# Optimization experiments

Hardware: AMD Instinct MI355X
Metric: run time of the kernel (lower is better)

Reference implementation:

```python
import jax, jax.numpy as jnp
import numpy as np

B, YS, XS, H = 16, 256, 256, 128  # batch, image height (y_size), width (x_size), MLP hidden


def setup_inputs() -> dict:
    key = jax.random.key(0)
    ks = jax.random.split(key, 6)
    images = jax.random.normal(ks[0], (B, YS, XS), dtype=jnp.float32)

    def glorot(k, shape):
        fan_in = shape[0]
        return (jax.random.normal(k, shape, dtype=jnp.float32) / np.float32(np.sqrt(fan_in)))

    W1 = glorot(ks[1], (3, H));  b1 = jnp.zeros((H,), jnp.float32)
    W2 = glorot(ks[2], (H, H));  b2 = jnp.zeros((H,), jnp.float32)
    W3 = glorot(ks[3], (H, H));  b3 = jnp.zeros((H,), jnp.float32)
    W4 = glorot(ks[4], (H, 1));  b4 = jnp.zeros((1,), jnp.float32)
    return {
        "images": images,
        "W1": W1, "b1": b1, "W2": W2, "b2": b2,
        "W3": W3, "b3": b3, "W4": W4, "b4": b4,
        "diffusion_weight": jnp.float32(0.1),
        "n": 0,
    }


def reference(images, W1, b1, W2, b2, W3, b3, W4, b4, diffusion_weight, n):
    # NOTE: in the original torch module, diffusion_loss (and all autograd
    # derivatives) are computed but never added to total_loss; only
    # boundary_loss accumulates. We reproduce exactly that math.
    Bn, y_size, x_size = images.shape
    x = jnp.linspace(-x_size / 2, x_size / 2, x_size, dtype=images.dtype)
    y = jnp.linspace(-y_size / 2, y_size / 2, y_size, dtype=images.dtype)
    Xg, Yg = jnp.meshgrid(x, y, indexing="ij")  # (x_size, y_size), x-major
    xf = Xg.ravel()  # (N,) with N = x_size*y_size
    yf = Yg.ravel()

    # t_recon is all-zeros in the original, so T_recon_i = i + n*B (constant field).
    ts = jnp.arange(Bn, dtype=images.dtype) + jnp.asarray(n * Bn, images.dtype)  # (B,)

    def field(tval):
        tf = jnp.zeros_like(xf) + tval
        inp = jnp.stack([xf, yf, tf], axis=-1)          # (N, 3)
        h = jnp.tanh(inp @ W1 + b1)
        h = jnp.tanh(h @ W2 + b2)
        h = jnp.tanh(h @ W3 + b3)
        return (h @ W4 + b4)[:, 0]                       # (N,)

    surface_recon = jax.vmap(field)(ts)                  # (B, N)
    # matches torch: surface_recon.view(y_size, x_size) on the ij-flattened field
    recon = surface_recon.reshape(Bn, y_size, x_size)
    boundary = jnp.mean((images - recon) ** 2, axis=(1, 2))  # per-sample
    return jnp.sum(boundary) / Bn
```

## Files before the change

### kernel.cpp

```cpp
#include <hip/hip_runtime.h>
#include <hip/hip_bf16.h>


#define BATCH 16
#define LDA 136
#define STEP (256.0f / 255.0f)
#define KS 2.8853900817779268f

typedef __bf16 v8bf __attribute__((ext_vector_type(8)));
typedef float  v4f  __attribute__((ext_vector_type(4)));

__device__ __forceinline__ unsigned short f2bf(float f) {
    unsigned int u = __float_as_uint(f);
    unsigned int r = (u + 0x7fffu + ((u >> 16) & 1u)) >> 16;
    return (unsigned short)r;
}

#if __has_builtin(__builtin_amdgcn_perm)
__device__ __forceinline__ unsigned int pack2bf(float a, float b) {
    return __builtin_amdgcn_perm(__float_as_uint(b), __float_as_uint(a), 0x07060302u);
}
#else
__device__ __forceinline__ unsigned int pack2bf(float a, float b) {
    return (__float_as_uint(a) >> 16) | (__float_as_uint(b) & 0xffff0000u);
}
#endif

__device__ __forceinline__ float tanh_pre(float zk) {
    float e = __builtin_amdgcn_exp2f(zk);
    float r = __builtin_amdgcn_rcpf(e + 1.f);
    return fmaf(-2.f, r, 1.f);
}

__global__ __launch_bounds__(256) void prep_kernel(
    const float* __restrict__ W2, const float* __restrict__ W3,
    unsigned short* __restrict__ w2t, unsigned short* __restrict__ w3t,
    float* __restrict__ partials, unsigned int* __restrict__ counter)
{
    int o = blockIdx.x * 256 + threadIdx.x;
    if (o < 1024) partials[o] = 0.f;
    if (o == 0) *counter = 0u;
    const float* src = (o < 16384) ? W2 : W3;
    unsigned short* dst = (o < 16384) ? w2t : w3t;
    int e = o & 16383;
    int k = e >> 7, n = e & 127;
    dst[n * 128 + k] = f2bf(src[e] * KS);
}

__global__ __launch_bounds__(512, 8) void main_kernel(
    const float* __restrict__ images,
    const float* __restrict__ W1, const float* __restrict__ b1,
    const float* __restrict__ b2, const float* __restrict__ b3,
    const float* __restrict__ W4, const float* __restrict__ b4,
    const int*   __restrict__ np,
    const unsigned short* __restrict__ w2t,
    const unsigned short* __restrict__ w3t,
    float* __restrict__ partials, unsigned int* __restrict__ counter,
    float* __restrict__ out)
{
    __shared__ unsigned short A[128 * LDA];
    __shared__ float P[8][128];
    __shared__ float red[8];
    __shared__ unsigned int isLastS;

    const int tid  = threadIdx.x;
    const int lane = tid & 63;
    const int w    = tid >> 6;
    const int l15  = lane & 15;
    const int quad = lane >> 4;

    const int bid = blockIdx.x;
    const int b   = bid >> 9;
    const int rem = bid & 511;
    const int r   = rem >> 1;
    const int c0  = (rem & 1) << 7;

    const float tv = (float)(b + np[0] * BATCH);
    const float xv = -128.f + (float)r * STEP;

    {
        const int lo = tid & 31, hi = tid >> 5;
        const int j0 = lo * 4, p0 = hi * 8;
        float4 wx = *(const float4*)(W1 + j0);
        float4 wy = *(const float4*)(W1 + 128 + j0);
        float4 wt = *(const float4*)(W1 + 256 + j0);
        float4 bb = *(const float4*)(b1 + j0);
        float wy0 = KS * wy.x, wy1 = KS * wy.y, wy2 = KS * wy.z, wy3 = KS * wy.w;
        const float yv0 = fmaf((float)(c0 + p0), STEP, -128.f);
        float z0 = fmaf(yv0, wy0, KS * fmaf(xv, wx.x, fmaf(tv, wt.x, bb.x)));
        float z1 = fmaf(yv0, wy1, KS * fmaf(xv, wx.y, fmaf(tv, wt.y, bb.y)));
        float z2 = fmaf(yv0, wy2, KS * fmaf(xv, wx.z, fmaf(tv, wt.z, bb.z)));
        float z3 = fmaf(yv0, wy3, KS * fmaf(xv, wx.w, fmaf(tv, wt.w, bb.w)));
        const float d0 = STEP * wy0, d1 = STEP * wy1, d2 = STEP * wy2, d3 = STEP * wy3;
        #pragma unroll
        for (int pi = 0; pi < 8; ++pi) {
            uint2 u = make_uint2(pack2bf(tanh_pre(z0), tanh_pre(z1)),
                                 pack2bf(tanh_pre(z2), tanh_pre(z3)));
            *(uint2*)&A[(p0 + pi) * LDA + j0] = u;
            z0 += d0; z1 += d1; z2 += d2; z3 += d3;
        }
    }
    __syncthreads();

    const int colw = w * 16 + l15;
    const int ch4  = w * 16 + quad * 4;

    v8bf wf[4];
    #pragma unroll
    for (int ks = 0; ks < 4; ++ks)
        wf[ks] = *(const v8bf*)(w2t + colw * 128 + ks * 32 + quad * 8);

    v4f acc[8];
    {
        float4 b2q = *(const float4*)(b2 + ch4);
        v4f ini = (v4f){b2q.x * KS, b2q.y * KS, b2q.z * KS, b2q.w * KS};
        #pragma unroll
        for (int mt = 0; mt < 8; ++mt) acc[mt] = ini;
    }
    #pragma unroll
    for (int ks = 0; ks < 4; ++ks) {
        #pragma unroll
        for (int mt = 0; mt < 8; ++mt) {
            v8bf af = *(const v8bf*)&A[(mt * 16 + l15) * LDA + ks * 32 + quad * 8];
            acc[mt] = __builtin_amdgcn_mfma_f32_16x16x32_bf16(wf[ks], af, acc[mt], 0, 0, 0);
        }
    }

    #pragma unroll
    for (int ks = 0; ks < 4; ++ks)
        wf[ks] = *(const v8bf*)(w3t + colw * 128 + ks * 32 + quad * 8);
    __syncthreads();

    #pragma unroll
    for (int mt = 0; mt < 8; ++mt) {
        uint2 u = make_uint2(pack2bf(tanh_pre(acc[mt][0]), tanh_pre(acc[mt][1])),
                             pack2bf(tanh_pre(acc[mt][2]), tanh_pre(acc[mt][3])));
        *(uint2*)&A[(mt * 16 + l15) * LDA + ch4] = u;
    }
    __syncthreads();

    {
        float4 b3q = *(const float4*)(b3 + ch4);
        v4f ini = (v4f){b3q.x * KS, b3q.y * KS, b3q.z * KS, b3q.w * KS};
        #pragma unroll
        for (int mt = 0; mt < 8; ++mt) acc[mt] = ini;
    }
    #pragma unroll
    for (int ks = 0; ks < 4; ++ks) {
        #pragma unroll
        for (int mt = 0; mt < 8; ++mt) {
            v8bf af = *(const v8bf*)&A[(mt * 16 + l15) * LDA + ks * 32 + quad * 8];
            acc[mt] = __builtin_amdgcn_mfma_f32_16x16x32_bf16(wf[ks], af, acc[mt], 0, 0, 0);
        }
    }

    {
        float4 w4q = *(const float4*)(W4 + ch4);
        #pragma unroll
        for (int mt = 0; mt < 8; ++mt) {
            float s;
            s  = tanh_pre(acc[mt][0]) * w4q.x;
            s  = fmaf(tanh_pre(acc[mt][1]), w4q.y, s);
            s  = fmaf(tanh_pre(acc[mt][2]), w4q.z, s);
            s  = fmaf(tanh_pre(acc[mt][3]), w4q.w, s);
            s += __shfl_xor(s, 16, 64);
            s += __shfl_xor(s, 32, 64);
            if (quad == 0) P[w][mt * 16 + l15] = s;
        }
    }
    __syncthreads();

    {
        float e2 = 0.f;
        if (tid < 128) {
            float s = b4[0];
            #pragma unroll
            for (int ww = 0; ww < 8; ++ww) s += P[ww][tid];
            float img = images[(b << 16) + (r << 8) + c0 + tid];
            float err = img - s;
            e2 = err * err;
        }
        #pragma unroll
        for (int off = 1; off < 64; off <<= 1)
            e2 += __shfl_xor(e2, off, 64);
        if (lane == 0 && tid < 128)
            atomicAdd(&partials[bid & 1023], e2);
    }

    __syncthreads();
    if (tid == 0)
        isLastS = (atomicAdd(counter, 1u) == (unsigned)(gridDim.x - 1)) ? 1u : 0u;
    __syncthreads();
    if (isLastS) {
        float s = __hip_atomic_load(&partials[tid],       __ATOMIC_RELAXED, __HIP_MEMORY_SCOPE_AGENT)
                + __hip_atomic_load(&partials[tid + 512], __ATOMIC_RELAXED, __HIP_MEMORY_SCOPE_AGENT);
        #pragma unroll
        for (int off = 1; off < 64; off <<= 1)
            s += __shfl_xor(s, off, 64);
        if (lane == 0) red[w] = s;
        __syncthreads();
        if (tid == 0) {
            float tot = 0.f;
            #pragma unroll
            for (int i = 0; i < 8; ++i) tot += red[i];
            out[0] = tot * (1.f / 1048576.f);
        }
    }
}

extern "C" void kernel_launch(void* const* d_in, const int* in_sizes, int n_in,
                              void* d_out, int out_size, void* d_ws, size_t ws_size,
                              hipStream_t stream)
{
    const float* images = (const float*)d_in[0];
    const float* W1 = (const float*)d_in[1];
    const float* b1 = (const float*)d_in[2];
    const float* W2 = (const float*)d_in[3];
    const float* b2 = (const float*)d_in[4];
    const float* W3 = (const float*)d_in[5];
    const float* b3 = (const float*)d_in[6];
    const float* W4 = (const float*)d_in[7];
    const float* b4 = (const float*)d_in[8];
    const int*   np = (const int*)d_in[10];

    unsigned short* w2t = (unsigned short*)d_ws;
    unsigned short* w3t = w2t + 128 * 128;
    float* partials = (float*)((char*)d_ws + 65536);
    unsigned int* counter = (unsigned int*)((char*)d_ws + 65536 + 4096);

    prep_kernel<<<128, 256, 0, stream>>>(W2, W3, w2t, w3t, partials, counter);
    main_kernel<<<BATCH * 256 * 2, 512, 0, stream>>>(
        images, W1, b1, b2, b3, W4, b4, np, w2t, w3t, partials, counter, (float*)d_out);
}
```

Baseline: 200.6 us.

## Switch hidden-layer GEMMs to 32x32x16 MFMA with 2D wave tiling

After: 235.1 us. 1.17x slower.

```diff
diff --git a/kernel.cpp b/kernel.cpp
--- a/kernel.cpp
+++ b/kernel.cpp
@@ -8,7 +8,7 @@
 #define KS 2.8853900817779268f
 
 typedef __bf16 v8bf __attribute__((ext_vector_type(8)));
-typedef float  v4f  __attribute__((ext_vector_type(4)));
+typedef float  v16f __attribute__((ext_vector_type(16)));
 
 __device__ __forceinline__ unsigned short f2bf(float f) {
     unsigned int u = __float_as_uint(f);
@@ -59,15 +59,18 @@
     float* __restrict__ out)
 {
     __shared__ unsigned short A[128 * LDA];
-    __shared__ float P[8][128];
+    __shared__ float P[4][128];
     __shared__ float red[8];
     __shared__ unsigned int isLastS;
 
     const int tid  = threadIdx.x;
     const int lane = tid & 63;
     const int w    = tid >> 6;
-    const int l15  = lane & 15;
-    const int quad = lane >> 4;
+    const int i32  = lane & 31;
+    const int h    = lane >> 5;
+
+    const int chb  = (w & 3) * 32;
+    const int ptb  = (w >> 2) * 64;
 
     const int bid = blockIdx.x;
     const int b   = bid >> 9;
@@ -102,70 +105,103 @@
     }
     __syncthreads();
 
-    const int colw = w * 16 + l15;
-    const int ch4  = w * 16 + quad * 4;
-
-    v8bf wf[4];
+    const int ch0 = chb + 4 * h;
+
+    const unsigned short* wb2 = w2t + (chb + i32) * 128 + h * 8;
+    v16f acc0, acc1;
+    {
+        float4 g0 = *(const float4*)(b2 + ch0);
+        float4 g1 = *(const float4*)(b2 + ch0 + 8);
+        float4 g2 = *(const float4*)(b2 + ch0 + 16);
+        float4 g3 = *(const float4*)(b2 + ch0 + 24);
+        acc0 = (v16f){g0.x*KS, g0.y*KS, g0.z*KS, g0.w*KS,
+                      g1.x*KS, g1.y*KS, g1.z*KS, g1.w*KS,
+                      g2.x*KS, g2.y*KS, g2.z*KS, g2.w*KS,
+                      g3.x*KS, g3.y*KS, g3.z*KS, g3.w*KS};
+        acc1 = acc0;
+    }
+    {
+        v8bf wcur = *(const v8bf*)(wb2);
+        #pragma unroll
+        for (int ks = 0; ks < 8; ++ks) {
+            v8bf wnext = (ks < 7) ? *(const v8bf*)(wb2 + (ks + 1) * 16) : wcur;
+            v8bf af0 = *(const v8bf*)&A[(ptb + i32)      * LDA + ks * 16 + h * 8];
+            v8bf af1 = *(const v8bf*)&A[(ptb + 32 + i32) * LDA + ks * 16 + h * 8];
+            acc0 = __builtin_amdgcn_mfma_f32_32x32x16_bf16(wcur, af0, acc0, 0, 0, 0);
+            acc1 = __builtin_amdgcn_mfma_f32_32x32x16_bf16(wcur, af1, acc1, 0, 0, 0);
+            wcur = wnext;
+        }
+    }
+    __syncthreads();
+
     #pragma unroll
-    for (int ks = 0; ks < 4; ++ks)
-        wf[ks] = *(const v8bf*)(w2t + colw * 128 + ks * 32 + quad * 8);
-
-    v4f acc[8];
-    {
-        float4 b2q = *(const float4*)(b2 + ch4);
-        v4f ini = (v4f){b2q.x * KS, b2q.y * KS, b2q.z * KS, b2q.w * KS};
-        #pragma unroll
-        for (int mt = 0; mt < 8; ++mt) acc[mt] = ini;
-    }
-    #pragma unroll
-    for (int ks = 0; ks < 4; ++ks) {
-        #pragma unroll
-        for (int mt = 0; mt < 8; ++mt) {
-            v8bf af = *(const v8bf*)&A[(mt * 16 + l15) * LDA + ks * 32 + quad * 8];
-            acc[mt] = __builtin_amdgcn_mfma_f32_16x16x32_bf16(wf[ks], af, acc[mt], 0, 0, 0);
-        }
-    }
-
-    #pragma unroll
-    for (int ks = 0; ks < 4; ++ks)
-        wf[ks] = *(const v8bf*)(w3t + colw * 128 + ks * 32 + quad * 8);
-    __syncthreads();
-
-    #pragma unroll
-    for (int mt = 0; mt < 8; ++mt) {
-        uint2 u = make_uint2(pack2bf(tanh_pre(acc[mt][0]), tanh_pre(acc[mt][1])),
-                             pack2bf(tanh_pre(acc[mt][2]), tanh_pre(acc[mt][3])));
-        *(uint2*)&A[(mt * 16 + l15) * LDA + ch4] = u;
-    }
-    __syncthreads();
-
-    {
-        float4 b3q = *(const float4*)(b3 + ch4);
-        v4f ini = (v4f){b3q.x * KS, b3q.y * KS, b3q.z * KS, b3q.w * KS};
-        #pragma unroll
-        for (int mt = 0; mt < 8; ++mt) acc[mt] = ini;
-    }
-    #pragma unroll
-    for (int ks = 0; ks < 4; ++ks) {
-        #pragma unroll
-        for (int mt = 0; mt < 8; ++mt) {
-            v8bf af = *(const v8bf*)&A[(mt * 16 + l15) * LDA + ks * 32 + quad * 8];
-            acc[mt] = __builtin_amdgcn_mfma_f32_16x16x32_bf16(wf[ks], af, acc[mt], 0, 0, 0);
-        }
-    }
-
-    {
-        float4 w4q = *(const float4*)(W4 + ch4);
-        #pragma unroll
-        for (int mt = 0; mt < 8; ++mt) {
+    for (int t = 0; t < 2; ++t) {
+        const v16f& ac = t ? acc1 : acc0;
+        const int prow = (ptb + t * 32 + i32) * LDA;
+        #pragma unroll
+        for (int g = 0; g < 4; ++g) {
+            float t0 = tanh_pre(ac[4 * g + 0]);
+            float t1 = tanh_pre(ac[4 * g + 1]);
+            float t2 = tanh_pre(ac[4 * g + 2]);
+            float t3 = tanh_pre(ac[4 * g + 3]);
+            uint2 u = make_uint2(pack2bf(t0, t1), pack2bf(t2, t3));
+            *(uint2*)&A[prow + ch0 + 8 * g] = u;
+        }
+    }
+    __syncthreads();
+
+    const unsigned short* wb3 = w3t + (chb + i32) * 128 + h * 8;
+    {
+        float4 g0 = *(const float4*)(b3 + ch0);
+        float4 g1 = *(const float4*)(b3 + ch0 + 8);
+        float4 g2 = *(const float4*)(b3 + ch0 + 16);
+        float4 g3 = *(const float4*)(b3 + ch0 + 24);
+        acc0 = (v16f){g0.x*KS, g0.y*KS, g0.z*KS, g0.w*KS,
+                      g1.x*KS, g1.y*KS, g1.z*KS, g1.w*KS,
+                      g2.x*KS, g2.y*KS, g2.z*KS, g2.w*KS,
+                      g3.x*KS, g3.y*KS, g3.z*KS, g3.w*KS};
+        acc1 = acc0;
+    }
+    {
+        v8bf wcur = *(const v8bf*)(wb3);
+        #pragma unroll
+        for (int ks = 0; ks < 8; ++ks) {
+            v8bf wnext = (ks < 7) ? *(const v8bf*)(wb3 + (ks + 1) * 16) : wcur;
+            v8bf af0 = *(const v8bf*)&A[(ptb + i32)      * LDA + ks * 16 + h * 8];
+            v8bf af1 = *(const v8bf*)&A[(ptb + 32 + i32) * LDA + ks * 16 + h * 8];
+            acc0 = __builtin_amdgcn_mfma_f32_32x32x16_bf16(wcur, af0, acc0, 0, 0, 0);
+            acc1 = __builtin_amdgcn_mfma_f32_32x32x16_bf16(wcur, af1, acc1, 0, 0, 0);
+            wcur = wnext;
+        }
+    }
+
+    {
+        float4 w40 = *(const float4*)(W4 + ch0);
+        float4 w41 = *(const float4*)(W4 + ch0 + 8);
+        float4 w42 = *(const float4*)(W4 + ch0 + 16);
+        float4 w43 = *(const float4*)(W4 + ch0 + 24);
+        #pragma unroll
+        for (int t = 0; t < 2; ++t) {
+            const v16f& ac = t ? acc1 : acc0;
             float s;
-            s  = tanh_pre(acc[mt][0]) * w4q.x;
-            s  = fmaf(tanh_pre(acc[mt][1]), w4q.y, s);
-            s  = fmaf(tanh_pre(acc[mt][2]), w4q.z, s);
-            s  = fmaf(tanh_pre(acc[mt][3]), w4q.w, s);
-            s += __shfl_xor(s, 16, 64);
+            s  = tanh_pre(ac[0])  * w40.x;
+            s  = fmaf(tanh_pre(ac[1]),  w40.y, s);
+            s  = fmaf(tanh_pre(ac[2]),  w40.z, s);
+            s  = fmaf(tanh_pre(ac[3]),  w40.w, s);
+            s  = fmaf(tanh_pre(ac[4]),  w41.x, s);
+            s  = fmaf(tanh_pre(ac[5]),  w41.y, s);
+            s  = fmaf(tanh_pre(ac[6]),  w41.z, s);
+            s  = fmaf(tanh_pre(ac[7]),  w41.w, s);
+            s  = fmaf(tanh_pre(ac[8]),  w42.x, s);
+            s  = fmaf(tanh_pre(ac[9]),  w42.y, s);
+            s  = fmaf(tanh_pre(ac[10]), w42.z, s);
+            s  = fmaf(tanh_pre(ac[11]), w42.w, s);
+            s  = fmaf(tanh_pre(ac[12]), w43.x, s);
+            s  = fmaf(tanh_pre(ac[13]), w43.y, s);
+            s  = fmaf(tanh_pre(ac[14]), w43.z, s);
+            s  = fmaf(tanh_pre(ac[15]), w43.w, s);
             s += __shfl_xor(s, 32, 64);
-            if (quad == 0) P[w][mt * 16 + l15] = s;
+            if (h == 0) P[w & 3][ptb + t * 32 + i32] = s;
         }
     }
     __syncthreads();
@@ -173,9 +209,7 @@
     {
         float e2 = 0.f;
         if (tid < 128) {
-            float s = b4[0];
-            #pragma unroll
-            for (int ww = 0; ww < 8; ++ww) s += P[ww][tid];
+            float s = b4[0] + P[0][tid] + P[1][tid] + P[2][tid] + P[3][tid];
             float img = images[(b << 16) + (r << 8) + c0 + tid];
             float err = img - s;
             e2 = err * err;
```
